# Performance work log

Measured on AMD Instinct MI355X. Metric: run time of the kernel, lower is better.

Reference implementation:

```python
import jax, jax.numpy as jnp
import numpy as np

B, N, F_IN, F_OUT, H = 8, 1024, 256, 256, 4
HD = F_OUT // H  # head_dim = 64
NEG_SLOPE = 0.2


def setup_inputs() -> dict:
    key = jax.random.key(0)
    k1, k2, k3 = jax.random.split(key, 3)
    x = jax.random.normal(k1, (B, N, F_IN), dtype=jnp.float32)
    adj = jnp.ones((B, N, N), dtype=jnp.int32)
    # Linear weight, stored as [in, out] so h = x @ W
    W = jax.random.normal(k2, (F_IN, F_OUT), dtype=jnp.float32) / np.sqrt(F_IN)
    # attention vector a: [H, 2*head_dim], xavier-ish init
    a = jax.random.normal(k3, (H, 2 * HD), dtype=jnp.float32) * np.sqrt(2.0 / (H + 2 * HD))
    return {"x": x, "adj": adj, "W": W, "a": a}


def reference(x, adj, W, a):
    Bq, Nq, _ = x.shape
    h = (x @ W).reshape(Bq, Nq, H, HD).transpose(0, 2, 1, 3)  # [B,H,N,HD]
    a1, a2 = a[:, :HD], a[:, HD:]  # decompose concat: e_nm = h_n.a1 + h_m.a2
    s1 = jnp.einsum('bhnd,hd->bhn', h, a1)
    s2 = jnp.einsum('bhmd,hd->bhm', h, a2)
    e = jax.nn.leaky_relu(s1[:, :, :, None] + s2[:, :, None, :], NEG_SLOPE)  # [B,H,N,N]
    e = jnp.where(adj[:, None, :, :] == 0, -jnp.inf, e)
    attention = jax.nn.softmax(e, axis=-1)
    out = jnp.einsum('bhnm,bhmd->bhnd', attention, h)
    return out.transpose(0, 2, 1, 3).reshape(Bq, Nq, H * HD)
```

## Files before the change

### kernel.cpp

```cpp
#include <hip/hip_runtime.h>
#include <math.h>

#define H 4
#define HD 64
#define NN 1024
#define BB 8
#define FIN 256
#define FOUT 256

typedef _Float16 f16x8 __attribute__((ext_vector_type(8)));
typedef _Float16 f16x4 __attribute__((ext_vector_type(4)));
typedef _Float16 f16x2 __attribute__((ext_vector_type(2)));
typedef float f32x4 __attribute__((ext_vector_type(4)));

__global__ __launch_bounds__(256) void wtrans(const float* __restrict__ W,
                                              _Float16* __restrict__ WT) {
  __shared__ float tile[64][68];
  const int tid = threadIdx.x;
  const int k0 = (blockIdx.x & 3) * 64, f0 = (blockIdx.x >> 2) * 64;
  const int r = tid >> 4, c4 = (tid & 15) * 4;
#pragma unroll
  for (int p = 0; p < 4; ++p) {
    float4 v = *(const float4*)&W[(size_t)(k0 + p * 16 + r) * FOUT + f0 + c4];
    *(float4*)&tile[p * 16 + r][c4] = v;
  }
  __syncthreads();
  const int f = tid >> 2, kg = (tid & 3) * 16;
#pragma unroll
  for (int i = 0; i < 4; ++i) {
    f16x4 o;
#pragma unroll
    for (int j = 0; j < 4; ++j) o[j] = (_Float16)tile[kg + i * 4 + j][f];
    *(f16x4*)&WT[(size_t)(f0 + f) * FIN + k0 + kg + i * 4] = o;
  }
}

__global__ __launch_bounds__(256) void gemm_xw(const float* __restrict__ x,
                                               const _Float16* __restrict__ WT,
                                               const float* __restrict__ a,
                                               _Float16* __restrict__ hT,
                                               float* __restrict__ s1_ws,
                                               float* __restrict__ s2_ws,
                                               float* __restrict__ u_ws,
                                               float* __restrict__ v_ws) {
  __shared__ _Float16 xs[64][264];
  const int tid = threadIdx.x;
  const int lane = tid & 63, w = tid >> 6;
  const int c = lane & 15, q = lane >> 4;
  const int bn0 = blockIdx.x * 64;
  const int head = blockIdx.y;
  const int b = bn0 >> 10, nb = bn0 & 1023;
  const int bh = b * H + head;

#pragma unroll
  for (int p = 0; p < 16; ++p) {
    int f = p * 256 + tid;
    int row = f >> 6, col = (f & 63) * 4;
    float4 v = *(const float4*)&x[(size_t)(bn0 + row) * FIN + col];
    f16x4 h4;
    h4[0] = (_Float16)v.x; h4[1] = (_Float16)v.y;
    h4[2] = (_Float16)v.z; h4[3] = (_Float16)v.w;
    *(f16x4*)&xs[row][col] = h4;
  }
  __syncthreads();

  f32x4 acc[4];
#pragma unroll
  for (int t = 0; t < 4; ++t) acc[t] = (f32x4){0.f, 0.f, 0.f, 0.f};
  const _Float16* wbase = WT + (size_t)head * 64 * FIN;
#pragma unroll
  for (int ks = 0; ks < 8; ++ks) {
    f16x8 af = *(const f16x8*)&xs[w * 16 + c][ks * 32 + q * 8];
#pragma unroll
    for (int t = 0; t < 4; ++t) {
      f16x8 bf = *(const f16x8*)&wbase[(size_t)(t * 16 + c) * FIN + ks * 32 + q * 8];
      acc[t] = __builtin_amdgcn_mfma_f32_16x16x32_f16(af, bf, acc[t], 0, 0, 0);
    }
  }

  float a1v[4], a2v[4];
#pragma unroll
  for (int t = 0; t < 4; ++t) {
    a1v[t] = a[head * 2 * HD + t * 16 + c];
    a2v[t] = a[head * 2 * HD + HD + t * 16 + c];
  }
  float s1p[4] = {0.f, 0.f, 0.f, 0.f};
  float s2p[4] = {0.f, 0.f, 0.f, 0.f};
#pragma unroll
  for (int t = 0; t < 4; ++t) {
    f16x4 hv;
#pragma unroll
    for (int rr = 0; rr < 4; ++rr) {
      hv[rr] = (_Float16)acc[t][rr];
      s1p[rr] += acc[t][rr] * a1v[t];
      s2p[rr] += acc[t][rr] * a2v[t];
    }
    *(f16x4*)&hT[((size_t)(bh * 64 + t * 16 + c)) * NN + nb + w * 16 + q * 4] = hv;
  }
#pragma unroll
  for (int rr = 0; rr < 4; ++rr) {
    float s1 = s1p[rr], s2 = s2p[rr];
#pragma unroll
    for (int off = 8; off; off >>= 1) {
      s1 += __shfl_xor(s1, off);
      s2 += __shfl_xor(s2, off);
    }
    if (c == 0) {
      int n = nb + w * 16 + q * 4 + rr;
      size_t idx = (size_t)bh * NN + n;
      s1_ws[idx] = s1;
      s2_ws[idx] = s2;
      u_ws[idx] = __expf(s2);
      v_ws[idx] = __expf(0.2f * s2);
    }
  }
}

__global__ __launch_bounds__(256) void attn(const _Float16* __restrict__ hT,
                                            const float* __restrict__ s1_ws,
                                            const float* __restrict__ s2_ws,
                                            const float* __restrict__ u_ws,
                                            const float* __restrict__ v_ws,
                                            const int* __restrict__ adj,
                                            float* __restrict__ out) {
  __shared__ float s2r[NN], uu[NN], vv[NN];
  __shared__ _Float16 pt[2][32][136];
  __shared__ float invL[32];
  const int tid = threadIdx.x, lane = tid & 63, w = tid >> 6;
  const int c = lane & 15, q = lane >> 4;
  const int ntile = blockIdx.x, bh = blockIdx.y;
  const int b = bh >> 2, head = bh & 3;
  const int n0 = ntile * 32;

  {
    size_t base = (size_t)bh * NN + tid * 4;
    *(float4*)&s2r[tid * 4] = *(const float4*)&s2_ws[base];
    *(float4*)&uu[tid * 4] = *(const float4*)&u_ws[base];
    *(float4*)&vv[tid * 4] = *(const float4*)&v_ws[base];
  }
  __syncthreads();

  float s1v[8];
#pragma unroll
  for (int r = 0; r < 8; ++r) s1v[r] = s1_ws[(size_t)bh * NN + n0 + w * 8 + r];

  float mx[8];
  unsigned msk[8];
#pragma unroll
  for (int r = 0; r < 8; ++r) { mx[r] = -INFINITY; msk[r] = 0u; }
  const int* adjp = adj + ((size_t)(b * NN + n0 + w * 8)) * NN + 2 * lane;
#pragma unroll
  for (int ch = 0; ch < 8; ++ch) {
    int2 av[8];
#pragma unroll
    for (int r = 0; r < 8; ++r) av[r] = *(const int2*)(adjp + (size_t)r * NN + ch * 128);
    float2 s2p = *(const float2*)&s2r[ch * 128 + 2 * lane];
#pragma unroll
    for (int r = 0; r < 8; ++r) {
      bool e0 = av[r].x != 0, e1 = av[r].y != 0;
      msk[r] |= (e0 ? (1u << (2 * ch)) : 0u) | (e1 ? (2u << (2 * ch)) : 0u);
      mx[r] = fmaxf(mx[r], e0 ? s2p.x : -INFINITY);
      mx[r] = fmaxf(mx[r], e1 ? s2p.y : -INFINITY);
    }
  }
  float Arow[8], Brow[8], ns1[8];
#pragma unroll
  for (int r = 0; r < 8; ++r) {
    float m = mx[r];
#pragma unroll
    for (int off = 32; off; off >>= 1) m = fmaxf(m, __shfl_xor(m, off));
    float t0 = s1v[r] + m;
    float M = fmaxf(t0, 0.2f * t0);
    Arow[r] = __expf(s1v[r] - M);
    Brow[r] = __expf(0.2f * s1v[r] - M);
    ns1[r] = -s1v[r];
  }

  float Lp[8];
#pragma unroll
  for (int r = 0; r < 8; ++r) Lp[r] = 0.f;
  f32x4 acc[2];
  acc[0] = (f32x4){0.f, 0.f, 0.f, 0.f};
  acc[1] = (f32x4){0.f, 0.f, 0.f, 0.f};
  const _Float16* bptr = hT + ((size_t)bh * 64 + w * 16 + c) * NN + q * 8;

  for (int ch = 0; ch < 8; ++ch) {
    const int buf = ch & 1;
    f16x8 bf0 = *(const f16x8*)(bptr + ch * 128);
    f16x8 bf1 = *(const f16x8*)(bptr + ch * 128 + 32);
    f16x8 bf2 = *(const f16x8*)(bptr + ch * 128 + 64);
    f16x8 bf3 = *(const f16x8*)(bptr + ch * 128 + 96);
    float2 s2p = *(const float2*)&s2r[ch * 128 + 2 * lane];
    float2 up = *(const float2*)&uu[ch * 128 + 2 * lane];
    float2 vp = *(const float2*)&vv[ch * 128 + 2 * lane];
#pragma unroll
    for (int r = 0; r < 8; ++r) {
      bool m0 = (msk[r] >> (2 * ch)) & 1u;
      bool m1 = (msk[r] >> (2 * ch + 1)) & 1u;
      float p0 = (s2p.x >= ns1[r]) ? Arow[r] * up.x : Brow[r] * vp.x;
      float p1 = (s2p.y >= ns1[r]) ? Arow[r] * up.y : Brow[r] * vp.y;
      p0 = m0 ? p0 : 0.f;
      p1 = m1 ? p1 : 0.f;
      Lp[r] += p0 + p1;
      f16x2 pk = __builtin_bit_cast(f16x2, __builtin_amdgcn_cvt_pkrtz(p0, p1));
      *(f16x2*)&pt[buf][w * 8 + r][2 * lane] = pk;
    }
    __syncthreads();
#pragma unroll
    for (int t = 0; t < 2; ++t) {
      f16x8 a0 = *(const f16x8*)&pt[buf][t * 16 + c][q * 8];
      f16x8 a1 = *(const f16x8*)&pt[buf][t * 16 + c][32 + q * 8];
      f16x8 a2 = *(const f16x8*)&pt[buf][t * 16 + c][64 + q * 8];
      f16x8 a3 = *(const f16x8*)&pt[buf][t * 16 + c][96 + q * 8];
      acc[t] = __builtin_amdgcn_mfma_f32_16x16x32_f16(a0, bf0, acc[t], 0, 0, 0);
      acc[t] = __builtin_amdgcn_mfma_f32_16x16x32_f16(a1, bf1, acc[t], 0, 0, 0);
      acc[t] = __builtin_amdgcn_mfma_f32_16x16x32_f16(a2, bf2, acc[t], 0, 0, 0);
      acc[t] = __builtin_amdgcn_mfma_f32_16x16x32_f16(a3, bf3, acc[t], 0, 0, 0);
    }
  }

  float myL = 0.f;
#pragma unroll
  for (int r = 0; r < 8; ++r) {
    float s = Lp[r];
#pragma unroll
    for (int off = 32; off; off >>= 1) s += __shfl_xor(s, off);
    if (lane == r) myL = s;
  }
  if (lane < 8) invL[w * 8 + lane] = 1.0f / myL;
  __syncthreads();
#pragma unroll
  for (int t = 0; t < 2; ++t) {
#pragma unroll
    for (int rr = 0; rr < 4; ++rr) {
      int nloc = t * 16 + q * 4 + rr;
      out[((size_t)(b * NN + n0 + nloc)) * FOUT + head * 64 + w * 16 + c] =
          acc[t][rr] * invL[nloc];
    }
  }
}

extern "C" void kernel_launch(void* const* d_in, const int* in_sizes, int n_in,
                              void* d_out, int out_size, void* d_ws, size_t ws_size,
                              hipStream_t stream) {
  const float* x = (const float*)d_in[0];
  const int* adj = (const int*)d_in[1];
  const float* W = (const float*)d_in[2];
  const float* a = (const float*)d_in[3];
  float* out = (float*)d_out;

  char* ws = (char*)d_ws;
  _Float16* hT = (_Float16*)ws;
  _Float16* WT = (_Float16*)(ws + (size_t)4 * 1024 * 1024);
  float* s1_ws = (float*)(ws + (size_t)4 * 1024 * 1024 + 128 * 1024);
  float* s2_ws = s1_ws + (size_t)BB * H * NN;
  float* u_ws = s2_ws + (size_t)BB * H * NN;
  float* v_ws = u_ws + (size_t)BB * H * NN;

  wtrans<<<16, 256, 0, stream>>>(W, WT);
  gemm_xw<<<dim3(128, 4), 256, 0, stream>>>(x, WT, a, hT, s1_ws, s2_ws, u_ws, v_ws);
  attn<<<dim3(32, 32), 256, 0, stream>>>(hT, s1_ws, s2_ws, u_ws, v_ws, adj, out);
}
```

Baseline: 125.3 us.

## Pack adjacency into bitmask once and reuse across heads in attention

```diff
diff --git a/kernel.cpp b/kernel.cpp
--- a/kernel.cpp
+++ b/kernel.cpp
@@ -33,6 +33,24 @@
     for (int j = 0; j < 4; ++j) o[j] = (_Float16)tile[kg + i * 4 + j][f];
     *(f16x4*)&WT[(size_t)(f0 + f) * FIN + k0 + kg + i * 4] = o;
   }
+}
+
+__global__ __launch_bounds__(256) void adjpack(const int* __restrict__ adj,
+                                               unsigned* __restrict__ adjP) {
+  size_t widx = (size_t)blockIdx.x * 256 + threadIdx.x;
+  const int4* p = (const int4*)adj + widx * 8;
+  int4 v[8];
+#pragma unroll
+  for (int i = 0; i < 8; ++i) v[i] = p[i];
+  unsigned bits = 0;
+#pragma unroll
+  for (int i = 0; i < 8; ++i) {
+    bits |= (v[i].x != 0 ? 1u : 0u) << (4 * i);
+    bits |= (v[i].y != 0 ? 2u : 0u) << (4 * i);
+    bits |= (v[i].z != 0 ? 4u : 0u) << (4 * i);
+    bits |= (v[i].w != 0 ? 8u : 0u) << (4 * i);
+  }
+  adjP[widx] = bits;
 }
 
 __global__ __launch_bounds__(256) void gemm_xw(const float* __restrict__ x,
@@ -52,14 +70,20 @@
   const int b = bn0 >> 10, nb = bn0 & 1023;
   const int bh = b * H + head;
 
+  float4 v[16];
 #pragma unroll
   for (int p = 0; p < 16; ++p) {
     int f = p * 256 + tid;
     int row = f >> 6, col = (f & 63) * 4;
-    float4 v = *(const float4*)&x[(size_t)(bn0 + row) * FIN + col];
+    v[p] = *(const float4*)&x[(size_t)(bn0 + row) * FIN + col];
+  }
+#pragma unroll
+  for (int p = 0; p < 16; ++p) {
+    int f = p * 256 + tid;
+    int row = f >> 6, col = (f & 63) * 4;
     f16x4 h4;
-    h4[0] = (_Float16)v.x; h4[1] = (_Float16)v.y;
-    h4[2] = (_Float16)v.z; h4[3] = (_Float16)v.w;
+    h4[0] = (_Float16)v[p].x; h4[1] = (_Float16)v[p].y;
+    h4[2] = (_Float16)v[p].z; h4[3] = (_Float16)v[p].w;
     *(f16x4*)&xs[row][col] = h4;
   }
   __syncthreads();
@@ -121,10 +145,11 @@
                                             const float* __restrict__ s2_ws,
                                             const float* __restrict__ u_ws,
                                             const float* __restrict__ v_ws,
-                                            const int* __restrict__ adj,
+                                            const unsigned* __restrict__ adjP,
                                             float* __restrict__ out) {
   __shared__ float s2r[NN], uu[NN], vv[NN];
   __shared__ _Float16 pt[2][32][136];
+  __shared__ unsigned adjW[32][32];
   __shared__ float invL[32];
   const int tid = threadIdx.x, lane = tid & 63, w = tid >> 6;
   const int c = lane & 15, q = lane >> 4;
@@ -137,6 +162,8 @@
     *(float4*)&s2r[tid * 4] = *(const float4*)&s2_ws[base];
     *(float4*)&uu[tid * 4] = *(const float4*)&u_ws[base];
     *(float4*)&vv[tid * 4] = *(const float4*)&v_ws[base];
+    uint4 aw = *(const uint4*)&adjP[((size_t)(b * NN + n0)) * 32 + tid * 4];
+    *(uint4*)&adjW[tid >> 3][(tid * 4) & 31] = aw;
   }
   __syncthreads();
 
@@ -144,23 +171,20 @@
 #pragma unroll
   for (int r = 0; r < 8; ++r) s1v[r] = s1_ws[(size_t)bh * NN + n0 + w * 8 + r];
 
+  const int wc = lane >> 4;
+  const int shft = (2 * lane) & 31;
+
   float mx[8];
-  unsigned msk[8];
-#pragma unroll
-  for (int r = 0; r < 8; ++r) { mx[r] = -INFINITY; msk[r] = 0u; }
-  const int* adjp = adj + ((size_t)(b * NN + n0 + w * 8)) * NN + 2 * lane;
+#pragma unroll
+  for (int r = 0; r < 8; ++r) mx[r] = -INFINITY;
 #pragma unroll
   for (int ch = 0; ch < 8; ++ch) {
-    int2 av[8];
-#pragma unroll
-    for (int r = 0; r < 8; ++r) av[r] = *(const int2*)(adjp + (size_t)r * NN + ch * 128);
     float2 s2p = *(const float2*)&s2r[ch * 128 + 2 * lane];
 #pragma unroll
     for (int r = 0; r < 8; ++r) {
-      bool e0 = av[r].x != 0, e1 = av[r].y != 0;
-      msk[r] |= (e0 ? (1u << (2 * ch)) : 0u) | (e1 ? (2u << (2 * ch)) : 0u);
-      mx[r] = fmaxf(mx[r], e0 ? s2p.x : -INFINITY);
-      mx[r] = fmaxf(mx[r], e1 ? s2p.y : -INFINITY);
+      unsigned bits = adjW[w * 8 + r][ch * 4 + wc] >> shft;
+      mx[r] = fmaxf(mx[r], (bits & 1u) ? s2p.x : -INFINITY);
+      mx[r] = fmaxf(mx[r], (bits & 2u) ? s2p.y : -INFINITY);
     }
   }
   float Arow[8], Brow[8], ns1[8];
@@ -195,12 +219,11 @@
     float2 vp = *(const float2*)&vv[ch * 128 + 2 * lane];
 #pragma unroll
     for (int r = 0; r < 8; ++r) {
-      bool m0 = (msk[r] >> (2 * ch)) & 1u;
-      bool m1 = (msk[r] >> (2 * ch + 1)) & 1u;
+      unsigned bits = adjW[w * 8 + r][ch * 4 + wc] >> shft;
       float p0 = (s2p.x >= ns1[r]) ? Arow[r] * up.x : Brow[r] * vp.x;
       float p1 = (s2p.y >= ns1[r]) ? Arow[r] * up.y : Brow[r] * vp.y;
-      p0 = m0 ? p0 : 0.f;
-      p1 = m1 ? p1 : 0.f;
+      p0 = (bits & 1u) ? p0 : 0.f;
+      p1 = (bits & 2u) ? p1 : 0.f;
       Lp[r] += p0 + p1;
       f16x2 pk = __builtin_bit_cast(f16x2, __builtin_amdgcn_cvt_pkrtz(p0, p1));
       *(f16x2*)&pt[buf][w * 8 + r][2 * lane] = pk;
@@ -256,8 +279,10 @@
   float* s2_ws = s1_ws + (size_t)BB * H * NN;
   float* u_ws = s2_ws + (size_t)BB * H * NN;
   float* v_ws = u_ws + (size_t)BB * H * NN;
+  unsigned* adjP = (unsigned*)(v_ws + (size_t)BB * H * NN);
 
   wtrans<<<16, 256, 0, stream>>>(W, WT);
+  adjpack<<<1024, 256, 0, stream>>>(adj, adjP);
   gemm_xw<<<dim3(128, 4), 256, 0, stream>>>(x, WT, a, hT, s1_ws, s2_ws, u_ws, v_ws);
-  attn<<<dim3(32, 32), 256, 0, stream>>>(hT, s1_ws, s2_ws, u_ws, v_ws, adj, out);
-}
+  attn<<<dim3(32, 32), 256, 0, stream>>>(hT, s1_ws, s2_ws, u_ws, v_ws, adjP, out);
+}
```

Result: faster. 120.5 us (-3.8%).
